# Optimization experiments

Measured on AMD Instinct MI355X. Metric: run time of the kernel, lower is better.

## Reference

```python
import jax, jax.numpy as jnp
import numpy as np

N_ATOMS = 40000
N_EDGES = 640000
N_BASIS = 128    # n_atom_basis == n_filters
N_RBF = 20
N_LAYERS = 3
MAX_Z = 100
CUTOFF = 5.0


def _ssp(x):
    # shifted softplus: softplus(x) - log(2)
    return jax.nn.softplus(x) - jnp.log(2.0).astype(x.dtype)


def setup_inputs() -> dict:
    key = jax.random.key(0)
    ks = jax.random.split(key, 16)
    s = 0.05
    inp = {
        'atomic_numbers': jax.random.randint(ks[0], (N_ATOMS,), 0, MAX_Z),
        'r_ij': jax.random.normal(ks[1], (N_EDGES, 3), dtype=jnp.float32),
        'idx_i': jnp.sort(jax.random.randint(ks[2], (N_EDGES,), 0, N_ATOMS)),
        'idx_j': jax.random.randint(ks[3], (N_EDGES,), 0, N_ATOMS),
        # learned parameters (stacked over interaction blocks)
        'emb': jax.random.normal(ks[4], (MAX_Z, N_BASIS), dtype=jnp.float32) * s,
        'in2f_W': jax.random.normal(ks[5], (N_LAYERS, N_BASIS, N_BASIS), dtype=jnp.float32) * s,
        'filt_W1': jax.random.normal(ks[6], (N_LAYERS, N_RBF, N_BASIS), dtype=jnp.float32) * s,
        'filt_b1': jax.random.normal(ks[7], (N_LAYERS, N_BASIS), dtype=jnp.float32) * s,
        'filt_W2': jax.random.normal(ks[8], (N_LAYERS, N_BASIS, N_BASIS), dtype=jnp.float32) * s,
        'filt_b2': jax.random.normal(ks[9], (N_LAYERS, N_BASIS), dtype=jnp.float32) * s,
        'out_W1': jax.random.normal(ks[10], (N_LAYERS, N_BASIS, N_BASIS), dtype=jnp.float32) * s,
        'out_b1': jax.random.normal(ks[11], (N_LAYERS, N_BASIS), dtype=jnp.float32) * s,
        'out_W2': jax.random.normal(ks[12], (N_LAYERS, N_BASIS, N_BASIS), dtype=jnp.float32) * s,
        'out_b2': jax.random.normal(ks[13], (N_LAYERS, N_BASIS), dtype=jnp.float32) * s,
    }
    return inp


def reference(atomic_numbers, r_ij, idx_i, idx_j, emb, in2f_W,
              filt_W1, filt_b1, filt_W2, filt_b2,
              out_W1, out_b1, out_W2, out_b2):
    x = emb[atomic_numbers]                                   # [N, F]
    # pairwise distances and radial basis expansion (GaussianRBF)
    d_ij = jnp.linalg.norm(r_ij, axis=1)                      # [E]
    offsets = jnp.linspace(0.0, CUTOFF, N_RBF, dtype=d_ij.dtype)
    coeff = -0.5 / (offsets[1] - offsets[0]) ** 2
    f_ij = jnp.exp(coeff * (d_ij[:, None] - offsets[None, :]) ** 2)  # [E, n_rbf]
    # cosine cutoff
    rcut_ij = 0.5 * (jnp.cos(d_ij * jnp.pi / CUTOFF) + 1.0) * (d_ij < CUTOFF)
    for l in range(N_LAYERS):
        h = x @ in2f_W[l]                                     # in2f (no bias) [N, F]
        Wij = _ssp(f_ij @ filt_W1[l] + filt_b1[l]) @ filt_W2[l] + filt_b2[l]
        Wij = Wij * rcut_ij[:, None]                          # [E, F]
        msg = h[idx_j] * Wij                                  # gather + filter-multiply
        agg = jax.ops.segment_sum(msg, idx_i, num_segments=N_ATOMS)  # scatter-sum [N, F]
        v = _ssp(agg @ out_W1[l] + out_b1[l]) @ out_W2[l] + out_b2[l]
        x = x + v                                             # residual update
    return x
```

## Files before the change

kernel.cpp:

```cpp
#include <hip/hip_runtime.h>
#include <math.h>

#define N_ATOMS 40000
#define N_EDGES 640000
#define NB      128
#define NRBF    20
#define NLAYERS 3
#define CUTOFF  5.0f
#define DELTA   (CUTOFF / 19.0f)
#define RBF_COEFF (-0.5f / (DELTA * DELTA))
#define LN2F    0.69314718055994531f

#define KTAB    2048
#define TSCALE  ((float)KTAB / CUTOFF)
#define EPB     256
#define EBLKS   (N_EDGES / EPB)
#define TABBLKS 1025

typedef __attribute__((ext_vector_type(8))) short bf16x8;
typedef __attribute__((ext_vector_type(4))) short bf16x4;
typedef __attribute__((ext_vector_type(4))) float fx4;

__device__ __forceinline__ float ssp_f(float x) {
    return fmaxf(x, 0.f) + __logf(1.f + __expf(-fabsf(x))) - LN2F;
}

__device__ __forceinline__ unsigned short bf16_rne(float x) {
    unsigned u = __float_as_uint(x);
    unsigned r = u + 0x7fffu + ((u >> 16) & 1u);
    return (unsigned short)(r >> 16);
}

__device__ __forceinline__ float bfl(unsigned u) { return __uint_as_float(u << 16); }
__device__ __forceinline__ float bfh(unsigned u) { return __uint_as_float(u & 0xffff0000u); }


__device__ __forceinline__ void stage_A_f32(const float* __restrict__ A, int row0, int kc,
                                            short* Ah, int tid) {
    #pragma unroll
    for (int it = 0; it < 4; ++it) {
        int idx4 = tid + it * 256;
        int r = idx4 >> 4, kq = (idx4 & 15) << 2;
        float4 v = *(const float4*)(A + (size_t)(row0 + r) * NB + kc * 64 + kq);
        bf16x4 hs;
        const float* vf = (const float*)&v;
        #pragma unroll
        for (int j = 0; j < 4; ++j) hs[j] = (short)bf16_rne(vf[j]);
        int wi = r * 64 + (kq ^ ((r & 7) << 3));
        *(bf16x4*)(Ah + wi) = hs;
    }
}

template<int ZERO>
__device__ __forceinline__ void stage_A_agg(float* __restrict__ A, int row0, int kc,
                                            short* Ah, int tid) {
    #pragma unroll
    for (int it = 0; it < 4; ++it) {
        int idx4 = tid + it * 256;
        int r = idx4 >> 4, kq = (idx4 & 15) << 2;
        float* src = A + (size_t)(row0 + r) * NB + kc * 64 + kq;
        float4 v = *(const float4*)src;
        if (ZERO) *(float4*)src = make_float4(0.f, 0.f, 0.f, 0.f);
        bf16x4 hs;
        const float* vf = (const float*)&v;
        #pragma unroll
        for (int j = 0; j < 4; ++j) hs[j] = (short)bf16_rne(vf[j]);
        int wi = r * 64 + (kq ^ ((r & 7) << 3));
        *(bf16x4*)(Ah + wi) = hs;
    }
}

__device__ __forceinline__ void stage_A_emb(const float* __restrict__ emb,
                                            const int* __restrict__ z, int row0, int kc,
                                            short* Ah, int tid) {
    #pragma unroll
    for (int it = 0; it < 4; ++it) {
        int idx4 = tid + it * 256;
        int r = idx4 >> 4, kq = (idx4 & 15) << 2;
        int zr = z[row0 + r];
        float4 v = *(const float4*)(emb + (size_t)zr * NB + kc * 64 + kq);
        bf16x4 hs;
        const float* vf = (const float*)&v;
        #pragma unroll
        for (int j = 0; j < 4; ++j) hs[j] = (short)bf16_rne(vf[j]);
        int wi = r * 64 + (kq ^ ((r & 7) << 3));
        *(bf16x4*)(Ah + wi) = hs;
    }
}

__device__ __forceinline__ void stage_W(const short* __restrict__ imgh,
                                        short* Wh, int tid) {
    #pragma unroll
    for (int it = 0; it < 4; ++it) {
        int i = tid + it * 256;
        ((bf16x8*)Wh)[i] = ((const bf16x8*)imgh)[i];
    }
}

__device__ __forceinline__ void stage_W_f32(const float* __restrict__ W, int kc,
                                            short* Wh, int tid) {
    #pragma unroll
    for (int it = 0; it < 8; ++it) {
        int i = tid + it * 256;
        int kl = i >> 5;
        int c0 = (i & 31) << 2;
        float4 v = *(const float4*)(W + (size_t)(kc * 64 + kl) * NB + c0);
        const float* vf = (const float*)&v;
        #pragma unroll
        for (int j = 0; j < 4; ++j) {
            int col = c0 + j;
            Wh[col * 64 + (kl ^ ((col & 7) << 3))] = (short)bf16_rne(vf[j]);
        }
    }
}

__device__ __forceinline__ void g_compute(const short* AH, int choff,
                                          const short* Wh,
                                          int wr, int wc, int lane, fx4 acc[2][4]) {
    #pragma unroll
    for (int ks = 0; ks < 2; ++ks) {
        int kb = ks * 32 + (lane >> 4) * 8;
        bf16x8 a_h[2];
        #pragma unroll
        for (int s = 0; s < 2; ++s) {
            int r = wr + s * 16 + (lane & 15);
            int idx = choff + r * 64 + (kb ^ ((r & 7) << 3));
            a_h[s] = *(const bf16x8*)(AH + idx);
        }
        #pragma unroll
        for (int c = 0; c < 4; ++c) {
            int col = wc + c * 16 + (lane & 15);
            int idx = col * 64 + (kb ^ ((col & 7) << 3));
            bf16x8 b_h = *(const bf16x8*)(Wh + idx);
            #pragma unroll
            for (int s = 0; s < 2; ++s)
                acc[s][c] = __builtin_amdgcn_mfma_f32_16x16x32_bf16(a_h[s], b_h, acc[s][c], 0, 0, 0);
        }
    }
}

__device__ __forceinline__ void tab_pack_store(const float* tv, int tb, int tid,
                                               unsigned* __restrict__ TabW) {
    int half = tid >> 7, f = tid & 127;
    if (f < 64) {
        int rr = tb * 2 + half;
        unsigned pk = (unsigned)bf16_rne(tv[half * 128 + 2 * f])
                    | ((unsigned)bf16_rne(tv[half * 128 + 2 * f + 1]) << 16);
        TabW[((size_t)rr * 64 + f) * 2] = pk;
        if (rr > 0) TabW[((size_t)(rr - 1) * 64 + f) * 2 + 1] = pk;
    }
}

#define P0_GEMM 625
#define P0_ZERO 1250
#define P0_TAB  1025
#define P0_DST  625
#define P0_WPR  64
__global__ __launch_bounds__(256) void k_pre0(const int* __restrict__ z,
                                              const float* __restrict__ emb,
                                              const float* __restrict__ r_ij,
                                              const float* __restrict__ in2f,
                                              const float* __restrict__ oW1,
                                              const float* __restrict__ oW2,
                                              const float* __restrict__ fW1,
                                              const float* __restrict__ fb1,
                                              const float* __restrict__ fW2,
                                              const float* __restrict__ fb2,
                                              unsigned short* __restrict__ HB,
                                              unsigned* __restrict__ TabW,
                                              float* __restrict__ AGG,
                                              float* __restrict__ U,
                                              short* __restrict__ Wimg) {
    __shared__ short APOOL[12288];
    int bid = blockIdx.x, tid = threadIdx.x;

    if (bid < P0_GEMM) {
        short* Ah = APOOL;
        short* Wh = APOOL + 4096;
        int wave = tid >> 6, lane = tid & 63;
        int wr = (wave & 1) * 32, wc = (wave >> 1) * 64;
        int row0 = bid * 64;
        fx4 acc[2][4];
        #pragma unroll
        for (int s = 0; s < 2; ++s)
            #pragma unroll
            for (int c = 0; c < 4; ++c)
                acc[s][c] = (fx4){0.f, 0.f, 0.f, 0.f};
        for (int kc = 0; kc < 2; ++kc) {
            if (kc) __syncthreads();
            stage_A_emb(emb, z, row0, kc, Ah, tid);
            stage_W_f32(in2f, kc, Wh, tid);
            __syncthreads();
            g_compute(Ah, 0, Wh, wr, wc, lane, acc);
        }
        #pragma unroll
        for (int s = 0; s < 2; ++s)
            #pragma unroll
            for (int c = 0; c < 4; ++c) {
                int colg = wc + c * 16 + (lane & 15);
                #pragma unroll
                for (int reg = 0; reg < 4; ++reg) {
                    int rowg = row0 + wr + s * 16 + (lane >> 4) * 4 + reg;
                    HB[(size_t)rowg * NB + colg] = bf16_rne(acc[s][c][reg]);
                }
            }
    } else if (bid < P0_GEMM + P0_ZERO) {
        int base = (bid - P0_GEMM) * 4096 + tid * 16;
        float4 zv = make_float4(0.f, 0.f, 0.f, 0.f);
        float4* p = (float4*)(AGG + base);
        p[0] = zv; p[1] = zv; p[2] = zv; p[3] = zv;
    } else if (bid < P0_GEMM + P0_ZERO + P0_TAB) {
        int tb = bid - (P0_GEMM + P0_ZERO);
        int half = tid >> 7, f = tid & 127;
        int r = tb * 2 + half;
        float* tl = (float*)APOOL;
        float* tv = tl + 256;
        float val = 0.f;
        float d = (float)r * (CUTOFF / (float)KTAB);
        if (r < KTAB) {
            float a = fb1[f];
            #pragma unroll
            for (int q = 0; q < NRBF; ++q) {
                float dr = d - (float)q * DELTA;
                a += __expf(RBF_COEFF * dr * dr) * fW1[q * NB + f];
            }
            tl[half * NB + f] = ssp_f(a);
        }
        __syncthreads();
        if (r < KTAB) {
            float w = fb2[f];
            #pragma unroll 4
            for (int k = 0; k < NB; ++k) w += tl[half * NB + k] * fW2[k * NB + f];
            float rc = 0.5f * (__cosf(d * ((float)M_PI / CUTOFF)) + 1.f);
            val = w * rc;
        }
        tv[half * NB + f] = val;
        __syncthreads();
        tab_pack_store(tv, tb, tid, TabW);
    } else if (bid < P0_GEMM + P0_ZERO + P0_TAB + P0_DST) {
        int e = (bid - (P0_GEMM + P0_ZERO + P0_TAB)) * 1024 + tid * 4;
        const float4* rv = (const float4*)(r_ij + (size_t)e * 3);
        float4 a = rv[0], b = rv[1], c = rv[2];
        float d0 = sqrtf(a.x * a.x + a.y * a.y + a.z * a.z);
        float d1 = sqrtf(a.w * a.w + b.x * b.x + b.y * b.y);
        float d2 = sqrtf(b.z * b.z + b.w * b.w + c.x * c.x);
        float d3 = sqrtf(c.y * c.y + c.z * c.z + c.w * c.w);
        *(float4*)(U + e) = make_float4(d0 * TSCALE, d1 * TSCALE, d2 * TSCALE, d3 * TSCALE);
    } else {
        int b2 = bid - (P0_GEMM + P0_ZERO + P0_TAB + P0_DST);
        int w = 1 + (b2 >> 3), seg = b2 & 7;
        int layer = w / 3, which = w % 3;
        const float* W = (which == 0 ? in2f : which == 1 ? oW1 : oW2)
                         + (size_t)layer * NB * NB;
        short* hi = Wimg + (size_t)w * 16384;
        int i0 = seg * 2048;
        #pragma unroll
        for (int ofs = 0; ofs < 2048; ofs += 256) {
            int i = i0 + ofs + tid;
            int k = i >> 7, col = i & 127;
            int kc = k >> 6, kl = k & 63;
            hi[kc * 8192 + col * 64 + (kl ^ ((col & 7) << 3))] = (short)bf16_rne(W[i]);
        }
    }
}

__global__ __launch_bounds__(256) void k_edge(const float* __restrict__ U,
                                              const int* __restrict__ idx_i,
                                              const int* __restrict__ idx_j,
                                              const unsigned* __restrict__ HBv,
                                              const uint2* __restrict__ TabP,
                                              float* __restrict__ AGG,
                                              const float* __restrict__ nW1,
                                              const float* __restrict__ nb1,
                                              const float* __restrict__ nW2,
                                              const float* __restrict__ nb2,
                                              unsigned* __restrict__ TabN) {
    __shared__ float u_s[EPB];
    __shared__ int   i_s[EPB];
    __shared__ int   j_s[EPB];
    __shared__ float t_lds[256];
    __shared__ float tv_lds[256];
    int tid = threadIdx.x;
    int bid = blockIdx.x;

    if (bid >= EBLKS) {
        int tb = bid - EBLKS;
        int half = tid >> 7, f = tid & 127;
        int r = tb * 2 + half;
        float val = 0.f;
        float d = (float)r * (CUTOFF / (float)KTAB);
        if (r < KTAB) {
            float a = nb1[f];
            #pragma unroll
            for (int q = 0; q < NRBF; ++q) {
                float dr = d - (float)q * DELTA;
                a += __expf(RBF_COEFF * dr * dr) * nW1[q * NB + f];
            }
            t_lds[half * NB + f] = ssp_f(a);
        }
        __syncthreads();
        if (r < KTAB) {
            float w = nb2[f];
            #pragma unroll 4
            for (int k = 0; k < NB; ++k) w += t_lds[half * NB + k] * nW2[k * NB + f];
            float rc = 0.5f * (__cosf(d * ((float)M_PI / CUTOFF)) + 1.f);
            val = w * rc;
        }
        tv_lds[half * NB + f] = val;
        __syncthreads();
        tab_pack_store(tv_lds, tb, tid, TabN);
        return;
    }

    int e0 = bid * EPB;
    u_s[tid] = U[e0 + tid];
    i_s[tid] = idx_i[e0 + tid];
    j_s[tid] = idx_j[e0 + tid];
    __syncthreads();

    int wave = tid >> 6, lane = tid & 63;
    int wbase = wave << 6;

    float axA = 0.f, ayA = 0.f, axB = 0.f, ayB = 0.f;
    int curA = -1, curB = -1;
    int nfA = 0, nfB = 0;

    #pragma unroll 2
    for (int t = 0; t < 32; ++t) {
        int eA = wbase + t;
        int eB = wbase + 32 + t;
        float uA = u_s[eA], uB = u_s[eB];
        int   iaA = i_s[eA], iaB = i_s[eB];
        int   jaA = j_s[eA], jaB = j_s[eB];

        int kA = (int)uA; kA = (kA > KTAB) ? KTAB : kA;
        int kB = (int)uB; kB = (kB > KTAB) ? KTAB : kB;
        float frA = uA - (float)kA;
        float frB = uB - (float)kB;

        uint2 tpA = TabP[(size_t)kA * 64 + lane];
        uint2 tpB = TabP[(size_t)kB * 64 + lane];
        unsigned hqA = HBv[(size_t)jaA * 64 + lane];
        unsigned hqB = HBv[(size_t)jaB * 64 + lane];

        float w0A = fmaf(frA, bfl(tpA.y) - bfl(tpA.x), bfl(tpA.x));
        float w1A = fmaf(frA, bfh(tpA.y) - bfh(tpA.x), bfh(tpA.x));
        float w0B = fmaf(frB, bfl(tpB.y) - bfl(tpB.x), bfl(tpB.x));
        float w1B = fmaf(frB, bfh(tpB.y) - bfh(tpB.x), bfh(tpB.x));

        if (iaA != curA) {
            if (curA >= 0) {
                float* p = AGG + (size_t)curA * NB + 2 * lane;
                if (nfA == 0) { atomicAdd(p, axA); atomicAdd(p + 1, ayA); }
                else          { *(float2*)p = make_float2(axA, ayA); }
                ++nfA;
            }
            axA = 0.f; ayA = 0.f;
            curA = iaA;
        }
        axA = fmaf(bfl(hqA), w0A, axA);
        ayA = fmaf(bfh(hqA), w1A, ayA);

        if (iaB != curB) {
            if (curB >= 0) {
                float* p = AGG + (size_t)curB * NB + 2 * lane;
                if (nfB == 0) { atomicAdd(p, axB); atomicAdd(p + 1, ayB); }
                else          { *(float2*)p = make_float2(axB, ayB); }
                ++nfB;
            }
            axB = 0.f; ayB = 0.f;
            curB = iaB;
        }
        axB = fmaf(bfl(hqB), w0B, axB);
        ayB = fmaf(bfh(hqB), w1B, ayB);
    }
    if (curA >= 0) {
        float* p = AGG + (size_t)curA * NB + 2 * lane;
        atomicAdd(p, axA); atomicAdd(p + 1, ayA);
    }
    if (curB >= 0) {
        float* p = AGG + (size_t)curB * NB + 2 * lane;
        atomicAdd(p, axB); atomicAdd(p + 1, ayB);
    }
}

template<int FIRST, int LAST>
__global__ __launch_bounds__(256) void k_fuse(float* __restrict__ AGG,
                                              const short* __restrict__ img1,
                                              const float* __restrict__ b1,
                                              const short* __restrict__ img2,
                                              const float* __restrict__ b2,
                                              const short* __restrict__ img0n,
                                              const int* __restrict__ z,
                                              const float* __restrict__ emb,
                                              float* __restrict__ X,
                                              unsigned short* __restrict__ HB) {
    __shared__ short POOL[16384];
    short* Ah = POOL;
    short* Th = POOL;
    short* Wh = POOL + 8192;

    int tid = threadIdx.x;
    int wave = tid >> 6, lane = tid & 63;
    int wr = (wave & 1) * 32, wc = (wave >> 1) * 64;
    int row0 = blockIdx.x * 64;

    fx4 accT[2][4];
    #pragma unroll
    for (int s = 0; s < 2; ++s)
        #pragma unroll
        for (int c = 0; c < 4; ++c)
            accT[s][c] = (fx4){0.f, 0.f, 0.f, 0.f};
    for (int kc = 0; kc < 2; ++kc) {
        if (kc) __syncthreads();
        stage_A_agg<!LAST>(AGG, row0, kc, Ah, tid);
        stage_W(img1 + kc * 8192, Wh, tid);
        __syncthreads();
        g_compute(Ah, 0, Wh, wr, wc, lane, accT);
    }
    __syncthreads();

    #pragma unroll
    for (int s = 0; s < 2; ++s)
        #pragma unroll
        for (int c = 0; c < 4; ++c) {
            int colg = wc + c * 16 + (lane & 15);
            float bv = b1[colg];
            int kc2 = colg >> 6, kl = colg & 63;
            #pragma unroll
            for (int reg = 0; reg < 4; ++reg) {
                int rl = wr + s * 16 + (lane >> 4) * 4 + reg;
                float t = ssp_f(accT[s][c][reg] + bv);
                Th[kc2 * 4096 + rl * 64 + (kl ^ ((rl & 7) << 3))] = (short)bf16_rne(t);
            }
        }
    stage_W(img2, Wh, tid);
    __syncthreads();

    fx4 accV[2][4];
    #pragma unroll
    for (int s = 0; s < 2; ++s)
        #pragma unroll
        for (int c = 0; c < 4; ++c)
            accV[s][c] = (fx4){0.f, 0.f, 0.f, 0.f};
    g_compute(Th, 0, Wh, wr, wc, lane, accV);
    __syncthreads();
    stage_W(img2 + 8192, Wh, tid);
    __syncthreads();
    g_compute(Th, 4096, Wh, wr, wc, lane, accV);
    __syncthreads();

    #pragma unroll
    for (int s = 0; s < 2; ++s)
        #pragma unroll
        for (int c = 0; c < 4; ++c) {
            int colg = wc + c * 16 + (lane & 15);
            float bv = b2[colg];
            int kc2 = colg >> 6, kl = colg & 63;
            #pragma unroll
            for (int reg = 0; reg < 4; ++reg) {
                int rowg = row0 + wr + s * 16 + (lane >> 4) * 4 + reg;
                size_t o = (size_t)rowg * NB + colg;
                float xo;
                if (FIRST) xo = emb[(size_t)z[rowg] * NB + colg];
                else       xo = X[o];
                float xn = xo + accV[s][c][reg] + bv;
                X[o] = xn;
                if (!LAST) {
                    int rl = wr + s * 16 + (lane >> 4) * 4 + reg;
                    Th[kc2 * 4096 + rl * 64 + (kl ^ ((rl & 7) << 3))] = (short)bf16_rne(xn);
                }
            }
        }
    if (LAST) return;

    stage_W(img0n, Wh, tid);
    __syncthreads();
    fx4 accH[2][4];
    #pragma unroll
    for (int s = 0; s < 2; ++s)
        #pragma unroll
        for (int c = 0; c < 4; ++c)
            accH[s][c] = (fx4){0.f, 0.f, 0.f, 0.f};
    g_compute(Th, 0, Wh, wr, wc, lane, accH);
    __syncthreads();
    stage_W(img0n + 8192, Wh, tid);
    __syncthreads();
    g_compute(Th, 4096, Wh, wr, wc, lane, accH);

    #pragma unroll
    for (int s = 0; s < 2; ++s)
        #pragma unroll
        for (int c = 0; c < 4; ++c) {
            int colg = wc + c * 16 + (lane & 15);
            #pragma unroll
            for (int reg = 0; reg < 4; ++reg) {
                int rowg = row0 + wr + s * 16 + (lane >> 4) * 4 + reg;
                HB[(size_t)rowg * NB + colg] = bf16_rne(accH[s][c][reg]);
            }
        }
}

extern "C" void kernel_launch(void* const* d_in, const int* in_sizes, int n_in,
                              void* d_out, int out_size, void* d_ws, size_t ws_size,
                              hipStream_t stream) {
    const int*   z    = (const int*)  d_in[0];
    const float* rij  = (const float*)d_in[1];
    const int*   ii   = (const int*)  d_in[2];
    const int*   jj   = (const int*)  d_in[3];
    const float* emb  = (const float*)d_in[4];
    const float* in2f = (const float*)d_in[5];
    const float* fW1  = (const float*)d_in[6];
    const float* fb1  = (const float*)d_in[7];
    const float* fW2  = (const float*)d_in[8];
    const float* fb2  = (const float*)d_in[9];
    const float* oW1  = (const float*)d_in[10];
    const float* ob1  = (const float*)d_in[11];
    const float* oW2  = (const float*)d_in[12];
    const float* ob2  = (const float*)d_in[13];

    const int NXF = N_ATOMS * NB;

    float* X = (float*)d_out;
    unsigned short* HB   = (unsigned short*)d_ws;
    float*          AGG  = (float*)(HB + (size_t)NXF);
    float*          U    = AGG + (size_t)NXF;
    unsigned*       Tab0 = (unsigned*)(U + N_EDGES);
    unsigned*       Tab1 = Tab0 + (size_t)2050 * 128;
    short*          Wimg = (short*)(Tab1 + (size_t)2050 * 128);

    k_pre0<<<P0_GEMM + P0_ZERO + P0_TAB + P0_DST + P0_WPR, 256, 0, stream>>>(
        z, emb, rij, in2f, oW1, oW2,
        fW1, fb1, fW2, fb2, HB, Tab0, AGG, U, Wimg);

    for (int l = 0; l < NLAYERS; ++l) {
        unsigned* TabCur = (l & 1) ? Tab1 : Tab0;
        unsigned* TabNxt = (l & 1) ? Tab0 : Tab1;
        int ln = (l < NLAYERS - 1) ? l + 1 : 0;
        int grid_e = EBLKS + ((l < NLAYERS - 1) ? TABBLKS : 0);

        k_edge<<<grid_e, 256, 0, stream>>>(U, ii, jj,
                                           (const unsigned*)HB,
                                           (const uint2*)TabCur,
                                           AGG,
                                           fW1 + (size_t)ln * NRBF * NB,
                                           fb1 + (size_t)ln * NB,
                                           fW2 + (size_t)ln * NB * NB,
                                           fb2 + (size_t)ln * NB,
                                           TabNxt);

        const short* img1  = Wimg + (size_t)(l * 3 + 1) * 16384;
        const short* img2  = Wimg + (size_t)(l * 3 + 2) * 16384;
        const short* img0n = Wimg + (size_t)((l + 1 < NLAYERS ? (l + 1) * 3 : 3)) * 16384;

        if (l == 0)
            k_fuse<1, 0><<<N_ATOMS / 64, 256, 0, stream>>>(AGG, img1, ob1 + (size_t)l * NB,
                                                           img2, ob2 + (size_t)l * NB,
                                                           img0n, z, emb, X, HB);
        else if (l < NLAYERS - 1)
            k_fuse<0, 0><<<N_ATOMS / 64, 256, 0, stream>>>(AGG, img1, ob1 + (size_t)l * NB,
                                                           img2, ob2 + (size_t)l * NB,
                                                           img0n, z, emb, X, HB);
        else
            k_fuse<0, 1><<<N_ATOMS / 64, 256, 0, stream>>>(AGG, img1, ob1 + (size_t)l * NB,
                                                           img2, ob2 + (size_t)l * NB,
                                                           img0n, z, emb, X, HB);
    }
}
```

Before: 226.9 us.

## Use nearest-neighbor filter table and pack edge metadata into single words

The filter lookup table doubles to 4096 entries and switches from linear interpolation over paired entries to nearest-neighbor lookup of a single bf16 row, which halves table bytes per edge lookup and removes the interpolation arithmetic. Edge distance index, idx_i and idx_j are packed once into a uint2 per edge (16-bit atom indices), so the edge kernel loads one LDS word instead of three arrays. Table generation work doubles and accuracy now depends on table resolution, and the 16-bit index packing relies on the atom count fitting in 16 bits.

```diff
diff --git a/kernel.cpp b/kernel.cpp
--- a/kernel.cpp
+++ b/kernel.cpp
@@ -11,11 +11,11 @@
 #define RBF_COEFF (-0.5f / (DELTA * DELTA))
 #define LN2F    0.69314718055994531f
 
-#define KTAB    2048
+#define KTAB    4096
 #define TSCALE  ((float)KTAB / CUTOFF)
 #define EPB     256
 #define EBLKS   (N_EDGES / EPB)
-#define TABBLKS 1025
+#define TABBLKS 2049
 
 typedef __attribute__((ext_vector_type(8))) short bf16x8;
 typedef __attribute__((ext_vector_type(4))) short bf16x4;
@@ -34,22 +34,6 @@
 __device__ __forceinline__ float bfl(unsigned u) { return __uint_as_float(u << 16); }
 __device__ __forceinline__ float bfh(unsigned u) { return __uint_as_float(u & 0xffff0000u); }
 
-
-__device__ __forceinline__ void stage_A_f32(const float* __restrict__ A, int row0, int kc,
-                                            short* Ah, int tid) {
-    #pragma unroll
-    for (int it = 0; it < 4; ++it) {
-        int idx4 = tid + it * 256;
-        int r = idx4 >> 4, kq = (idx4 & 15) << 2;
-        float4 v = *(const float4*)(A + (size_t)(row0 + r) * NB + kc * 64 + kq);
-        bf16x4 hs;
-        const float* vf = (const float*)&v;
-        #pragma unroll
-        for (int j = 0; j < 4; ++j) hs[j] = (short)bf16_rne(vf[j]);
-        int wi = r * 64 + (kq ^ ((r & 7) << 3));
-        *(bf16x4*)(Ah + wi) = hs;
-    }
-}
 
 template<int ZERO>
 __device__ __forceinline__ void stage_A_agg(float* __restrict__ A, int row0, int kc,
@@ -139,26 +123,16 @@
     }
 }
 
-__device__ __forceinline__ void tab_pack_store(const float* tv, int tb, int tid,
-                                               unsigned* __restrict__ TabW) {
-    int half = tid >> 7, f = tid & 127;
-    if (f < 64) {
-        int rr = tb * 2 + half;
-        unsigned pk = (unsigned)bf16_rne(tv[half * 128 + 2 * f])
-                    | ((unsigned)bf16_rne(tv[half * 128 + 2 * f + 1]) << 16);
-        TabW[((size_t)rr * 64 + f) * 2] = pk;
-        if (rr > 0) TabW[((size_t)(rr - 1) * 64 + f) * 2 + 1] = pk;
-    }
-}
-
 #define P0_GEMM 625
 #define P0_ZERO 1250
-#define P0_TAB  1025
+#define P0_TAB  TABBLKS
 #define P0_DST  625
 #define P0_WPR  64
 __global__ __launch_bounds__(256) void k_pre0(const int* __restrict__ z,
                                               const float* __restrict__ emb,
                                               const float* __restrict__ r_ij,
+                                              const int* __restrict__ ii,
+                                              const int* __restrict__ jj,
                                               const float* __restrict__ in2f,
                                               const float* __restrict__ oW1,
                                               const float* __restrict__ oW2,
@@ -167,9 +141,9 @@
                                               const float* __restrict__ fW2,
                                               const float* __restrict__ fb2,
                                               unsigned short* __restrict__ HB,
-                                              unsigned* __restrict__ TabW,
+                                              unsigned short* __restrict__ TabB,
                                               float* __restrict__ AGG,
-                                              float* __restrict__ U,
+                                              uint2* __restrict__ PK,
                                               short* __restrict__ Wimg) {
     __shared__ short APOOL[12288];
     int bid = blockIdx.x, tid = threadIdx.x;
@@ -214,7 +188,6 @@
         int half = tid >> 7, f = tid & 127;
         int r = tb * 2 + half;
         float* tl = (float*)APOOL;
-        float* tv = tl + 256;
         float val = 0.f;
         float d = (float)r * (CUTOFF / (float)KTAB);
         if (r < KTAB) {
@@ -234,18 +207,28 @@
             float rc = 0.5f * (__cosf(d * ((float)M_PI / CUTOFF)) + 1.f);
             val = w * rc;
         }
-        tv[half * NB + f] = val;
-        __syncthreads();
-        tab_pack_store(tv, tb, tid, TabW);
+        TabB[(size_t)r * NB + f] = bf16_rne(val);
     } else if (bid < P0_GEMM + P0_ZERO + P0_TAB + P0_DST) {
         int e = (bid - (P0_GEMM + P0_ZERO + P0_TAB)) * 1024 + tid * 4;
         const float4* rv = (const float4*)(r_ij + (size_t)e * 3);
         float4 a = rv[0], b = rv[1], c = rv[2];
+        int4 iv = *(const int4*)(ii + e);
+        int4 jv = *(const int4*)(jj + e);
         float d0 = sqrtf(a.x * a.x + a.y * a.y + a.z * a.z);
         float d1 = sqrtf(a.w * a.w + b.x * b.x + b.y * b.y);
         float d2 = sqrtf(b.z * b.z + b.w * b.w + c.x * c.x);
         float d3 = sqrtf(c.y * c.y + c.z * c.z + c.w * c.w);
-        *(float4*)(U + e) = make_float4(d0 * TSCALE, d1 * TSCALE, d2 * TSCALE, d3 * TSCALE);
+        float u0 = fminf(d0 * TSCALE + 0.5f, (float)KTAB);
+        float u1 = fminf(d1 * TSCALE + 0.5f, (float)KTAB);
+        float u2 = fminf(d2 * TSCALE + 0.5f, (float)KTAB);
+        float u3 = fminf(d3 * TSCALE + 0.5f, (float)KTAB);
+        uint4 w0, w1;
+        w0.x = __float_as_uint(u0); w0.y = ((unsigned)iv.x << 16) | (unsigned)jv.x;
+        w0.z = __float_as_uint(u1); w0.w = ((unsigned)iv.y << 16) | (unsigned)jv.y;
+        w1.x = __float_as_uint(u2); w1.y = ((unsigned)iv.z << 16) | (unsigned)jv.z;
+        w1.z = __float_as_uint(u3); w1.w = ((unsigned)iv.w << 16) | (unsigned)jv.w;
+        *(uint4*)(PK + e) = w0;
+        *(uint4*)(PK + e + 2) = w1;
     } else {
         int b2 = bid - (P0_GEMM + P0_ZERO + P0_TAB + P0_DST);
         int w = 1 + (b2 >> 3), seg = b2 & 7;
@@ -264,22 +247,17 @@
     }
 }
 
-__global__ __launch_bounds__(256) void k_edge(const float* __restrict__ U,
-                                              const int* __restrict__ idx_i,
-                                              const int* __restrict__ idx_j,
+__global__ __launch_bounds__(256) void k_edge(const uint2* __restrict__ PK,
                                               const unsigned* __restrict__ HBv,
-                                              const uint2* __restrict__ TabP,
+                                              const unsigned* __restrict__ TabU,
                                               float* __restrict__ AGG,
                                               const float* __restrict__ nW1,
                                               const float* __restrict__ nb1,
                                               const float* __restrict__ nW2,
                                               const float* __restrict__ nb2,
-                                              unsigned* __restrict__ TabN) {
-    __shared__ float u_s[EPB];
-    __shared__ int   i_s[EPB];
-    __shared__ int   j_s[EPB];
+                                              unsigned short* __restrict__ TabN) {
+    __shared__ uint2 m_s[EPB];
     __shared__ float t_lds[256];
-    __shared__ float tv_lds[256];
     int tid = threadIdx.x;
     int bid = blockIdx.x;
 
@@ -306,16 +284,12 @@
             float rc = 0.5f * (__cosf(d * ((float)M_PI / CUTOFF)) + 1.f);
             val = w * rc;
         }
-        tv_lds[half * NB + f] = val;
-        __syncthreads();
-        tab_pack_store(tv_lds, tb, tid, TabN);
+        TabN[(size_t)r * NB + f] = bf16_rne(val);
         return;
     }
 
     int e0 = bid * EPB;
-    u_s[tid] = U[e0 + tid];
-    i_s[tid] = idx_i[e0 + tid];
-    j_s[tid] = idx_j[e0 + tid];
+    m_s[tid] = PK[e0 + tid];
     __syncthreads();
 
     int wave = tid >> 6, lane = tid & 63;
@@ -325,32 +299,24 @@
     int curA = -1, curB = -1;
     int nfA = 0, nfB = 0;
 
-    #pragma unroll 2
+    #pragma unroll 4
     for (int t = 0; t < 32; ++t) {
-        int eA = wbase + t;
-        int eB = wbase + 32 + t;
-        float uA = u_s[eA], uB = u_s[eB];
-        int   iaA = i_s[eA], iaB = i_s[eB];
-        int   jaA = j_s[eA], jaB = j_s[eB];
-
-        int kA = (int)uA; kA = (kA > KTAB) ? KTAB : kA;
-        int kB = (int)uB; kB = (kB > KTAB) ? KTAB : kB;
-        float frA = uA - (float)kA;
-        float frB = uB - (float)kB;
-
-        uint2 tpA = TabP[(size_t)kA * 64 + lane];
-        uint2 tpB = TabP[(size_t)kB * 64 + lane];
-        unsigned hqA = HBv[(size_t)jaA * 64 + lane];
-        unsigned hqB = HBv[(size_t)jaB * 64 + lane];
-
-        float w0A = fmaf(frA, bfl(tpA.y) - bfl(tpA.x), bfl(tpA.x));
-        float w1A = fmaf(frA, bfh(tpA.y) - bfh(tpA.x), bfh(tpA.x));
-        float w0B = fmaf(frB, bfl(tpB.y) - bfl(tpB.x), bfl(tpB.x));
-        float w1B = fmaf(frB, bfh(tpB.y) - bfh(tpB.x), bfh(tpB.x));
+        uint2 mA = m_s[wbase + t];
+        uint2 mB = m_s[wbase + 32 + t];
+
+        int kA = (int)__uint_as_float(mA.x);
+        int kB = (int)__uint_as_float(mB.x);
+        int iaA = (int)(mA.y >> 16), jaA = (int)(mA.y & 0xffffu);
+        int iaB = (int)(mB.y >> 16), jaB = (int)(mB.y & 0xffffu);
+
+        unsigned tvA = TabU[kA * 64 + lane];
+        unsigned tvB = TabU[kB * 64 + lane];
+        unsigned hqA = HBv[jaA * 64 + lane];
+        unsigned hqB = HBv[jaB * 64 + lane];
 
         if (iaA != curA) {
             if (curA >= 0) {
-                float* p = AGG + (size_t)curA * NB + 2 * lane;
+                float* p = AGG + curA * NB + 2 * lane;
                 if (nfA == 0) { atomicAdd(p, axA); atomicAdd(p + 1, ayA); }
                 else          { *(float2*)p = make_float2(axA, ayA); }
                 ++nfA;
@@ -358,12 +324,12 @@
             axA = 0.f; ayA = 0.f;
             curA = iaA;
         }
-        axA = fmaf(bfl(hqA), w0A, axA);
-        ayA = fmaf(bfh(hqA), w1A, ayA);
+        axA = fmaf(bfl(hqA), bfl(tvA), axA);
+        ayA = fmaf(bfh(hqA), bfh(tvA), ayA);
 
         if (iaB != curB) {
             if (curB >= 0) {
-                float* p = AGG + (size_t)curB * NB + 2 * lane;
+                float* p = AGG + curB * NB + 2 * lane;
                 if (nfB == 0) { atomicAdd(p, axB); atomicAdd(p + 1, ayB); }
                 else          { *(float2*)p = make_float2(axB, ayB); }
                 ++nfB;
@@ -371,15 +337,15 @@
             axB = 0.f; ayB = 0.f;
             curB = iaB;
         }
-        axB = fmaf(bfl(hqB), w0B, axB);
-        ayB = fmaf(bfh(hqB), w1B, ayB);
+        axB = fmaf(bfl(hqB), bfl(tvB), axB);
+        ayB = fmaf(bfh(hqB), bfh(tvB), ayB);
     }
     if (curA >= 0) {
-        float* p = AGG + (size_t)curA * NB + 2 * lane;
+        float* p = AGG + curA * NB + 2 * lane;
         atomicAdd(p, axA); atomicAdd(p + 1, ayA);
     }
     if (curB >= 0) {
-        float* p = AGG + (size_t)curB * NB + 2 * lane;
+        float* p = AGG + curB * NB + 2 * lane;
         atomicAdd(p, axB); atomicAdd(p + 1, ayB);
     }
 }
@@ -524,24 +490,24 @@
     float* X = (float*)d_out;
     unsigned short* HB   = (unsigned short*)d_ws;
     float*          AGG  = (float*)(HB + (size_t)NXF);
-    float*          U    = AGG + (size_t)NXF;
-    unsigned*       Tab0 = (unsigned*)(U + N_EDGES);
-    unsigned*       Tab1 = Tab0 + (size_t)2050 * 128;
-    short*          Wimg = (short*)(Tab1 + (size_t)2050 * 128);
+    uint2*          PK   = (uint2*)(AGG + (size_t)NXF);
+    unsigned short* Tab0 = (unsigned short*)(PK + N_EDGES);
+    unsigned short* Tab1 = Tab0 + (size_t)4098 * NB;
+    short*          Wimg = (short*)(Tab1 + (size_t)4098 * NB);
 
     k_pre0<<<P0_GEMM + P0_ZERO + P0_TAB + P0_DST + P0_WPR, 256, 0, stream>>>(
-        z, emb, rij, in2f, oW1, oW2,
-        fW1, fb1, fW2, fb2, HB, Tab0, AGG, U, Wimg);
+        z, emb, rij, ii, jj, in2f, oW1, oW2,
+        fW1, fb1, fW2, fb2, HB, Tab0, AGG, PK, Wimg);
 
     for (int l = 0; l < NLAYERS; ++l) {
-        unsigned* TabCur = (l & 1) ? Tab1 : Tab0;
-        unsigned* TabNxt = (l & 1) ? Tab0 : Tab1;
+        unsigned short* TabCur = (l & 1) ? Tab1 : Tab0;
+        unsigned short* TabNxt = (l & 1) ? Tab0 : Tab1;
         int ln = (l < NLAYERS - 1) ? l + 1 : 0;
         int grid_e = EBLKS + ((l < NLAYERS - 1) ? TABBLKS : 0);
 
-        k_edge<<<grid_e, 256, 0, stream>>>(U, ii, jj,
+        k_edge<<<grid_e, 256, 0, stream>>>(PK,
                                            (const unsigned*)HB,
-                                           (const uint2*)TabCur,
+                                           (const unsigned*)TabCur,
                                            AGG,
                                            fW1 + (size_t)ln * NRBF * NB,
                                            fb1 + (size_t)ln * NB,
```

Measured after the change: 232.9 us. 1.03x slower.

## Shrink filter lookup table to 256 rows with plain bf16 row layout

Applied to the files above, without the earlier changes.

The filter table over distance shrinks from 2048 to 256 samples, and the packed neighbor-pair layout (uint2 holding rows k and k+1) becomes a plain bf16 row-major table. The edge kernel now reads rows k and k+1 with two separate loads. A smaller table fits better in cache and needs fewer table-build blocks per layer, and dropping the LDS staging and extra sync removes the pair-packing step. The risk is extra interpolation error from linear interpolation on a coarser grid, plus one more load per edge.

```diff
diff --git a/kernel.cpp b/kernel.cpp
--- a/kernel.cpp
+++ b/kernel.cpp
@@ -11,11 +11,12 @@
 #define RBF_COEFF (-0.5f / (DELTA * DELTA))
 #define LN2F    0.69314718055994531f
 
-#define KTAB    2048
+#define KTAB    256
+#define TROWS   (KTAB + 2)
 #define TSCALE  ((float)KTAB / CUTOFF)
 #define EPB     256
 #define EBLKS   (N_EDGES / EPB)
-#define TABBLKS 1025
+#define TABBLKS (TROWS / 2)
 
 typedef __attribute__((ext_vector_type(8))) short bf16x8;
 typedef __attribute__((ext_vector_type(4))) short bf16x4;
@@ -34,22 +35,6 @@
 __device__ __forceinline__ float bfl(unsigned u) { return __uint_as_float(u << 16); }
 __device__ __forceinline__ float bfh(unsigned u) { return __uint_as_float(u & 0xffff0000u); }
 
-
-__device__ __forceinline__ void stage_A_f32(const float* __restrict__ A, int row0, int kc,
-                                            short* Ah, int tid) {
-    #pragma unroll
-    for (int it = 0; it < 4; ++it) {
-        int idx4 = tid + it * 256;
-        int r = idx4 >> 4, kq = (idx4 & 15) << 2;
-        float4 v = *(const float4*)(A + (size_t)(row0 + r) * NB + kc * 64 + kq);
-        bf16x4 hs;
-        const float* vf = (const float*)&v;
-        #pragma unroll
-        for (int j = 0; j < 4; ++j) hs[j] = (short)bf16_rne(vf[j]);
-        int wi = r * 64 + (kq ^ ((r & 7) << 3));
-        *(bf16x4*)(Ah + wi) = hs;
-    }
-}
 
 template<int ZERO>
 __device__ __forceinline__ void stage_A_agg(float* __restrict__ A, int row0, int kc,
@@ -139,21 +124,9 @@
     }
 }
 
-__device__ __forceinline__ void tab_pack_store(const float* tv, int tb, int tid,
-                                               unsigned* __restrict__ TabW) {
-    int half = tid >> 7, f = tid & 127;
-    if (f < 64) {
-        int rr = tb * 2 + half;
-        unsigned pk = (unsigned)bf16_rne(tv[half * 128 + 2 * f])
-                    | ((unsigned)bf16_rne(tv[half * 128 + 2 * f + 1]) << 16);
-        TabW[((size_t)rr * 64 + f) * 2] = pk;
-        if (rr > 0) TabW[((size_t)(rr - 1) * 64 + f) * 2 + 1] = pk;
-    }
-}
-
 #define P0_GEMM 625
 #define P0_ZERO 1250
-#define P0_TAB  1025
+#define P0_TAB  TABBLKS
 #define P0_DST  625
 #define P0_WPR  64
 __global__ __launch_bounds__(256) void k_pre0(const int* __restrict__ z,
@@ -167,7 +140,7 @@
                                               const float* __restrict__ fW2,
                                               const float* __restrict__ fb2,
                                               unsigned short* __restrict__ HB,
-                                              unsigned* __restrict__ TabW,
+                                              unsigned short* __restrict__ TabB,
                                               float* __restrict__ AGG,
                                               float* __restrict__ U,
                                               short* __restrict__ Wimg) {
@@ -214,7 +187,6 @@
         int half = tid >> 7, f = tid & 127;
         int r = tb * 2 + half;
         float* tl = (float*)APOOL;
-        float* tv = tl + 256;
         float val = 0.f;
         float d = (float)r * (CUTOFF / (float)KTAB);
         if (r < KTAB) {
@@ -234,9 +206,7 @@
             float rc = 0.5f * (__cosf(d * ((float)M_PI / CUTOFF)) + 1.f);
             val = w * rc;
         }
-        tv[half * NB + f] = val;
-        __syncthreads();
-        tab_pack_store(tv, tb, tid, TabW);
+        TabB[(size_t)r * NB + f] = bf16_rne(val);
     } else if (bid < P0_GEMM + P0_ZERO + P0_TAB + P0_DST) {
         int e = (bid - (P0_GEMM + P0_ZERO + P0_TAB)) * 1024 + tid * 4;
         const float4* rv = (const float4*)(r_ij + (size_t)e * 3);
@@ -268,18 +238,17 @@
                                               const int* __restrict__ idx_i,
                                               const int* __restrict__ idx_j,
                                               const unsigned* __restrict__ HBv,
-                                              const uint2* __restrict__ TabP,
+                                              const unsigned* __restrict__ TabU,
                                               float* __restrict__ AGG,
                                               const float* __restrict__ nW1,
                                               const float* __restrict__ nb1,
                                               const float* __restrict__ nW2,
                                               const float* __restrict__ nb2,
-                                              unsigned* __restrict__ TabN) {
+                                              unsigned short* __restrict__ TabN) {
     __shared__ float u_s[EPB];
     __shared__ int   i_s[EPB];
     __shared__ int   j_s[EPB];
     __shared__ float t_lds[256];
-    __shared__ float tv_lds[256];
     int tid = threadIdx.x;
     int bid = blockIdx.x;
 
@@ -306,9 +275,7 @@
             float rc = 0.5f * (__cosf(d * ((float)M_PI / CUTOFF)) + 1.f);
             val = w * rc;
         }
-        tv_lds[half * NB + f] = val;
-        __syncthreads();
-        tab_pack_store(tv_lds, tb, tid, TabN);
+        TabN[(size_t)r * NB + f] = bf16_rne(val);
         return;
     }
 
@@ -338,15 +305,17 @@
         float frA = uA - (float)kA;
         float frB = uB - (float)kB;
 
-        uint2 tpA = TabP[(size_t)kA * 64 + lane];
-        uint2 tpB = TabP[(size_t)kB * 64 + lane];
-        unsigned hqA = HBv[(size_t)jaA * 64 + lane];
-        unsigned hqB = HBv[(size_t)jaB * 64 + lane];
-
-        float w0A = fmaf(frA, bfl(tpA.y) - bfl(tpA.x), bfl(tpA.x));
-        float w1A = fmaf(frA, bfh(tpA.y) - bfh(tpA.x), bfh(tpA.x));
-        float w0B = fmaf(frB, bfl(tpB.y) - bfl(tpB.x), bfl(tpB.x));
-        float w1B = fmaf(frB, bfh(tpB.y) - bfh(tpB.x), bfh(tpB.x));
+        unsigned v0A = TabU[kA * 64 + lane];
+        unsigned v1A = TabU[kA * 64 + 64 + lane];
+        unsigned v0B = TabU[kB * 64 + lane];
+        unsigned v1B = TabU[kB * 64 + 64 + lane];
+        unsigned hqA = HBv[jaA * 64 + lane];
+        unsigned hqB = HBv[jaB * 64 + lane];
+
+        float w0A = fmaf(frA, bfl(v1A) - bfl(v0A), bfl(v0A));
+        float w1A = fmaf(frA, bfh(v1A) - bfh(v0A), bfh(v0A));
+        float w0B = fmaf(frB, bfl(v1B) - bfl(v0B), bfl(v0B));
+        float w1B = fmaf(frB, bfh(v1B) - bfh(v0B), bfh(v0B));
 
         if (iaA != curA) {
             if (curA >= 0) {
@@ -525,23 +494,23 @@
     unsigned short* HB   = (unsigned short*)d_ws;
     float*          AGG  = (float*)(HB + (size_t)NXF);
     float*          U    = AGG + (size_t)NXF;
-    unsigned*       Tab0 = (unsigned*)(U + N_EDGES);
-    unsigned*       Tab1 = Tab0 + (size_t)2050 * 128;
-    short*          Wimg = (short*)(Tab1 + (size_t)2050 * 128);
+    unsigned short* Tab0 = (unsigned short*)(U + N_EDGES);
+    unsigned short* Tab1 = Tab0 + (size_t)TROWS * NB;
+    short*          Wimg = (short*)(Tab1 + (size_t)TROWS * NB);
 
     k_pre0<<<P0_GEMM + P0_ZERO + P0_TAB + P0_DST + P0_WPR, 256, 0, stream>>>(
         z, emb, rij, in2f, oW1, oW2,
         fW1, fb1, fW2, fb2, HB, Tab0, AGG, U, Wimg);
 
     for (int l = 0; l < NLAYERS; ++l) {
-        unsigned* TabCur = (l & 1) ? Tab1 : Tab0;
-        unsigned* TabNxt = (l & 1) ? Tab0 : Tab1;
+        unsigned short* TabCur = (l & 1) ? Tab1 : Tab0;
+        unsigned short* TabNxt = (l & 1) ? Tab0 : Tab1;
         int ln = (l < NLAYERS - 1) ? l + 1 : 0;
         int grid_e = EBLKS + ((l < NLAYERS - 1) ? TABBLKS : 0);
 
         k_edge<<<grid_e, 256, 0, stream>>>(U, ii, jj,
                                            (const unsigned*)HB,
-                                           (const uint2*)TabCur,
+                                           (const unsigned*)TabCur,
                                            AGG,
                                            fW1 + (size_t)ln * NRBF * NB,
                                            fb1 + (size_t)ln * NB,
```

Result: faster. 214.5 us (-5.5%).
